# Performance work log

Measured on AMD Instinct MI355X. Metric: run time of the kernel, lower is better.

Reference implementation:

```python
import jax, jax.numpy as jnp
import numpy as np

NUM_NODES = 50000
NUM_EDGES = 800000
NUM_GRAPHS = 100
NODES_PER_GRAPH = 500
K = 250  # ceil(0.5 * NODES_PER_GRAPH), TopKPooling ratio=0.5
D = 64
OUT = 10


def gcn_conv(x, edge_index, W, b, num_nodes):
    """PyG GCNConv: add self-loops, symmetric D^-1/2 (A+I) D^-1/2 (x @ W) + b."""
    h = x @ W  # [N, Dout]
    loop = jnp.arange(num_nodes)
    row = jnp.concatenate([edge_index[0], loop])  # sources
    col = jnp.concatenate([edge_index[1], loop])  # targets
    deg = jax.ops.segment_sum(jnp.ones_like(col, dtype=h.dtype), col,
                              num_segments=num_nodes)
    dis = jnp.where(deg > 0, jax.lax.rsqrt(jnp.maximum(deg, 1e-12)), 0.0)
    norm = dis[row] * dis[col]                      # [E+N]
    msgs = h[row] * norm[:, None]                   # gather + scale (memory bound)
    out = jax.ops.segment_sum(msgs, col, num_segments=num_nodes)
    return out + b


def setup_inputs() -> dict:
    key = jax.random.key(0)
    ks = jax.random.split(key, 8)
    x = jax.random.normal(ks[0], (NUM_NODES, D), jnp.float32)
    edge_index = jax.random.randint(ks[1], (2, NUM_EDGES), 0, NUM_NODES)
    batch = jnp.arange(NUM_NODES) // NODES_PER_GRAPH  # contiguous equal graphs
    s = 1.0 / np.sqrt(D)
    W0 = jax.random.uniform(ks[2], (D, D), jnp.float32, -s, s)
    b0 = jnp.zeros((D,), jnp.float32)
    W1 = jax.random.uniform(ks[3], (D, D), jnp.float32, -s, s)
    b1 = jnp.zeros((D,), jnp.float32)
    pool_w = jax.random.uniform(ks[4], (D,), jnp.float32, -s, s)
    W_lin = jax.random.uniform(ks[5], (D, OUT), jnp.float32, -s, s)
    b_lin = jnp.zeros((OUT,), jnp.float32)
    return {"x": x, "edge_index": edge_index, "batch": batch,
            "W0": W0, "b0": b0, "W1": W1, "b1": b1,
            "pool_w": pool_w, "W_lin": W_lin, "b_lin": b_lin}


def reference(x, edge_index, batch, W0, b0, W1, b1, pool_w, W_lin, b_lin):
    # NOTE: zip(convs, pools) runs only 2 iterations -> 2 convs, 1 pool.
    x = jax.nn.relu(gcn_conv(x, edge_index, W0, b0, NUM_NODES))
    x = jax.nn.relu(gcn_conv(x, edge_index, W1, b1, NUM_NODES))
    # TopKPooling: score = tanh((x . w) / ||w||), keep top-K per graph,
    # kept features are scaled by their score.
    score = jnp.tanh((x @ pool_w) / jnp.linalg.norm(pool_w))  # [N]
    score_g = score.reshape(NUM_GRAPHS, NODES_PER_GRAPH)
    top_s, top_i = jax.lax.top_k(score_g, K)                  # [G, K]
    gidx = (top_i + jnp.arange(NUM_GRAPHS)[:, None] * NODES_PER_GRAPH).reshape(-1)
    x_pool = x[gidx] * top_s.reshape(-1, 1)                   # [G*K, D]
    # global_mean_pool: each pooled graph has exactly K nodes
    pooled = x_pool.reshape(NUM_GRAPHS, K, D).mean(axis=1)    # [G, D]
    logits = pooled @ W_lin + b_lin                           # [G, OUT]
    return jax.nn.log_softmax(logits, axis=1)
```

## Files before the change

kernel.cpp:

```cpp
#include <hip/hip_runtime.h>
#include <hip/hip_bf16.h>
#include <math.h>

#define NODES 50000
#define EDGES 800000
#define GRAPHS 100
#define NPG 500
#define KTOP 250
#define DIM 64
#define OUTC 10
#define SLOTS 64
#define GROWS 32
#define NBKT 196
#define BCAP 5120

#define WS_FLAG      0u
#define WS_INVNORM   4u
#define WS_W1F       512u
#define WS_B0F       16896u
#define WS_B1F       17152u
#define WS_PWF       17408u
#define WS_WLF       17664u
#define WS_BLF       20224u
#define WS_CURS      20480u
#define WS_CNT       21504u
#define WS_DIS       221696u
#define WS_SCORE     421888u
#define WS_EBUF      622080u
#define WS_SLOT      4636160u
#define WS_H1B       11036160u
#define WS_H2B       17436160u
#define WS_X2        23836160u

__device__ __forceinline__ float bf16_bits_to_f32(unsigned short u) {
    return __uint_as_float(((unsigned int)u) << 16);
}
__device__ __forceinline__ float bf16_lo(unsigned int u) {
    return __uint_as_float(u << 16);
}
__device__ __forceinline__ float bf16_hi(unsigned int u) {
    return __uint_as_float(u & 0xffff0000u);
}
__device__ __forceinline__ unsigned short f32_to_bf16(float f) {
    unsigned int u = __float_as_uint(f);
    u += 0x7fffu + ((u >> 16) & 1u);
    return (unsigned short)(u >> 16);
}
__device__ __forceinline__ unsigned int f32_sortable(float f) {
    unsigned int b = __float_as_uint(f);
    return (b & 0x80000000u) ? ~b : (b | 0x80000000u);
}

__global__ __launch_bounds__(512) void k_bucket(const int* __restrict__ ei,
        const void* w0p, const void* b0p, const void* w1p, const void* b1p,
        const void* pwp, const void* wlp, const void* blp, char* __restrict__ ws) {
    int bid = blockIdx.x, t = threadIdx.x;
    if (bid < NBKT) {
        __shared__ int hist[NBKT];
        __shared__ int base[NBKT];
        if (t < NBKT) hist[t] = 0;
        __syncthreads();
        int e0 = bid * 4096;
        int rr[8], cc[8], loc[8];
        long be = (long)e0 + (long)t * 8;
        if (be + 8 <= EDGES) {
            int4 ra = ((const int4*)(ei + e0))[t * 2];
            int4 rb = ((const int4*)(ei + e0))[t * 2 + 1];
            int4 ca = ((const int4*)(ei + EDGES + e0))[t * 2];
            int4 cb = ((const int4*)(ei + EDGES + e0))[t * 2 + 1];
            rr[0] = ra.x; rr[1] = ra.y; rr[2] = ra.z; rr[3] = ra.w;
            rr[4] = rb.x; rr[5] = rb.y; rr[6] = rb.z; rr[7] = rb.w;
            cc[0] = ca.x; cc[1] = ca.y; cc[2] = ca.z; cc[3] = ca.w;
            cc[4] = cb.x; cc[5] = cb.y; cc[6] = cb.z; cc[7] = cb.w;
        } else {
#pragma unroll
            for (int j = 0; j < 8; j++) {
                long e = be + j;
                if (e < EDGES) { rr[j] = ei[e]; cc[j] = ei[EDGES + e]; }
                else cc[j] = -1;
            }
        }
#pragma unroll
        for (int j = 0; j < 8; j++)
            if (cc[j] >= 0) loc[j] = atomicAdd(&hist[cc[j] >> 8], 1);
        __syncthreads();
        if (t < NBKT) base[t] = atomicAdd((int*)(ws + WS_CURS) + t, hist[t]);
        __syncthreads();
        unsigned int* eb = (unsigned int*)(ws + WS_EBUF);
#pragma unroll
        for (int j = 0; j < 8; j++) {
            if (cc[j] >= 0) {
                int b = cc[j] >> 8;
                int o = base[b] + loc[j];
                if (o < BCAP)
                    eb[b * BCAP + o] =
                        ((unsigned int)(cc[j] & 255) << 16) | (unsigned int)rr[j];
            }
        }
        return;
    }
    __shared__ int red_sh[512];
    __shared__ float fred[64];
    const unsigned short* u16 = (const unsigned short*)w0p;
    int c = 0;
    for (int i = t; i < 4096; i += 512) {
        float v = bf16_bits_to_f32(u16[i]);
        float av = fabsf(v);
        if (v == 0.0f || (av >= 1e-9f && av <= 0.25f)) c++;
    }
    red_sh[t] = c;
    __syncthreads();
    for (int s = 256; s > 0; s >>= 1) {
        if (t < s) red_sh[t] += red_sh[t + s];
        __syncthreads();
    }
    int flag = (red_sh[0] >= 3686) ? 1 : 0;
    if (t == 0) *(int*)(ws + WS_FLAG) = flag;
    const void* srcs[6] = {w1p, b0p, b1p, pwp, wlp, blp};
    const int   ns[6]   = {4096, 64, 64, 64, 640, 10};
    const unsigned int dsts[6] = {WS_W1F, WS_B0F, WS_B1F, WS_PWF, WS_WLF, WS_BLF};
    for (int a = 0; a < 6; a++) {
        float* dst = (float*)(ws + dsts[a]);
        if (flag) {
            const unsigned short* sp = (const unsigned short*)srcs[a];
            for (int i = t; i < ns[a]; i += 512) dst[i] = bf16_bits_to_f32(sp[i]);
        } else {
            const float* sp = (const float*)srcs[a];
            for (int i = t; i < ns[a]; i += 512) dst[i] = sp[i];
        }
    }
    __syncthreads();
    if (t < 64) {
        float w = ((float*)(ws + WS_PWF))[t];
        fred[t] = w * w;
    }
    __syncthreads();
    if (t == 0) {
        float ssum = 0.f;
        for (int i = 0; i < 64; i++) ssum += fred[i];
        *(float*)(ws + WS_INVNORM) = rsqrtf(ssum);
    }
}

__global__ __launch_bounds__(1024) void k_build(char* __restrict__ ws) {
    __shared__ unsigned short slsh[256 * SLOTS];
    __shared__ int cl_cnt[256];
    int b = blockIdx.x, t = threadIdx.x;
    if (t < 256) cl_cnt[t] = 0;
    __syncthreads();
    int n = ((const int*)(ws + WS_CURS))[b];
    if (n > BCAP) n = BCAP;
    const unsigned int* eb = (const unsigned int*)(ws + WS_EBUF) + b * BCAP;
    for (int i = t; i < n; i += 1024) {
        unsigned int u = eb[i];
        int cl = u >> 16;
        int r = u & 0xffffu;
        int p = atomicAdd(&cl_cnt[cl], 1);
        if (p < SLOTS) slsh[cl * SLOTS + p] = (unsigned short)r;
    }
    __syncthreads();
    uint4* dstv = (uint4*)((unsigned short*)(ws + WS_SLOT) + (b << 8) * SLOTS);
    const uint4* srcv = (const uint4*)slsh;
    for (int i = t; i < 2048; i += 1024) dstv[i] = srcv[i];
    if (t < 256) {
        int v = (b << 8) + t;
        if (v < NODES) {
            int cv = cl_cnt[t];
            ((int*)(ws + WS_CNT))[v] = cv;
            ((float*)(ws + WS_DIS))[v] = rsqrtf((float)(cv + 1));
        }
    }
}

__global__ __launch_bounds__(256) void k_gemm0(const void* __restrict__ xp,
        const void* __restrict__ w0p, char* __restrict__ ws,
        unsigned short* __restrict__ H1B) {
    __shared__ float Wsh[64 * 64];
    __shared__ float xsh[GROWS * 65];
    int bid = blockIdx.x, t = threadIdx.x;
    int flag = *(const int*)(ws + WS_FLAG);
    if (flag) {
        const unsigned short* wp = (const unsigned short*)w0p;
        for (int i = t; i < 4096; i += 256) Wsh[i] = bf16_bits_to_f32(wp[i]);
    } else {
        for (int i = t; i < 1024; i += 256)
            ((float4*)Wsh)[i] = ((const float4*)w0p)[i];
    }
    int row0 = bid * GROWS;
    for (int i = t; i < GROWS * 16; i += 256) {
        int r = i >> 4, q = i & 15;
        int gr = row0 + r;
        float4 v = {0.f, 0.f, 0.f, 0.f};
        if (gr < NODES) {
            if (flag) {
                ushort4 u = ((const ushort4*)xp)[gr * 16 + q];
                v.x = bf16_bits_to_f32(u.x); v.y = bf16_bits_to_f32(u.y);
                v.z = bf16_bits_to_f32(u.z); v.w = bf16_bits_to_f32(u.w);
            } else {
                v = ((const float4*)xp)[gr * 16 + q];
            }
        }
        float* xd = xsh + r * 65 + q * 4;
        xd[0] = v.x; xd[1] = v.y; xd[2] = v.z; xd[3] = v.w;
    }
    __syncthreads();
    int tc = t & 15, tr = t >> 4;
    int c0 = tc * 4, r0 = tr * 2;
    float4 a0 = {0, 0, 0, 0}, a1 = {0, 0, 0, 0};
#pragma unroll
    for (int k = 0; k < 64; k++) {
        float4 wv = *(const float4*)(Wsh + k * 64 + c0);
        float x0 = xsh[r0 * 65 + k];
        float x1 = xsh[(r0 + 1) * 65 + k];
        a0.x += wv.x * x0; a0.y += wv.y * x0; a0.z += wv.z * x0; a0.w += wv.w * x0;
        a1.x += wv.x * x1; a1.y += wv.y * x1; a1.z += wv.z * x1; a1.w += wv.w * x1;
    }
    int gr0 = row0 + r0;
    ushort4 s0, s1;
    s0.x = f32_to_bf16(a0.x); s0.y = f32_to_bf16(a0.y);
    s0.z = f32_to_bf16(a0.z); s0.w = f32_to_bf16(a0.w);
    s1.x = f32_to_bf16(a1.x); s1.y = f32_to_bf16(a1.y);
    s1.z = f32_to_bf16(a1.z); s1.w = f32_to_bf16(a1.w);
    if (gr0 < NODES)     *(ushort4*)(H1B + gr0 * 64 + c0) = s0;
    if (gr0 + 1 < NODES) *(ushort4*)(H1B + (gr0 + 1) * 64 + c0) = s1;
}

__device__ __forceinline__ void agg_core(const unsigned short* __restrict__ HB,
        const char* __restrict__ ws, int v, int eg, int dh,
        const float* bias, float4& olo, float4& ohi, float& dvo) {
    const int* cnt = (const int*)(ws + WS_CNT);
    const unsigned short* slot = (const unsigned short*)(ws + WS_SLOT) + v * SLOTS;
    const float* dis = (const float*)(ws + WS_DIS);
    int deg = cnt[v];
    if (deg > SLOTS) deg = SLOTS;
    float dv = dis[v];
    dvo = dv;
    float4 alo = {0, 0, 0, 0}, ahi = {0, 0, 0, 0};
    float4 blo = {0, 0, 0, 0}, bhi = {0, 0, 0, 0};
    if (eg == 0) {
        uint4 u = *(const uint4*)(HB + v * 64 + dh * 8);
        alo.x = bf16_lo(u.x) * dv; alo.y = bf16_hi(u.x) * dv;
        alo.z = bf16_lo(u.y) * dv; alo.w = bf16_hi(u.y) * dv;
        ahi.x = bf16_lo(u.z) * dv; ahi.y = bf16_hi(u.z) * dv;
        ahi.z = bf16_lo(u.w) * dv; ahi.w = bf16_hi(u.w) * dv;
    }
    int e = eg;
    for (; e + 8 < deg; e += 16) {
        int sA = slot[e], sB = slot[e + 8];
        float dA = dis[sA], dB = dis[sB];
        uint4 uA = *(const uint4*)(HB + sA * 64 + dh * 8);
        uint4 uB = *(const uint4*)(HB + sB * 64 + dh * 8);
        alo.x += bf16_lo(uA.x) * dA; alo.y += bf16_hi(uA.x) * dA;
        alo.z += bf16_lo(uA.y) * dA; alo.w += bf16_hi(uA.y) * dA;
        ahi.x += bf16_lo(uA.z) * dA; ahi.y += bf16_hi(uA.z) * dA;
        ahi.z += bf16_lo(uA.w) * dA; ahi.w += bf16_hi(uA.w) * dA;
        blo.x += bf16_lo(uB.x) * dB; blo.y += bf16_hi(uB.x) * dB;
        blo.z += bf16_lo(uB.y) * dB; blo.w += bf16_hi(uB.y) * dB;
        bhi.x += bf16_lo(uB.z) * dB; bhi.y += bf16_hi(uB.z) * dB;
        bhi.z += bf16_lo(uB.w) * dB; bhi.w += bf16_hi(uB.w) * dB;
    }
    if (e < deg) {
        int sA = slot[e];
        float dA = dis[sA];
        uint4 uA = *(const uint4*)(HB + sA * 64 + dh * 8);
        alo.x += bf16_lo(uA.x) * dA; alo.y += bf16_hi(uA.x) * dA;
        alo.z += bf16_lo(uA.y) * dA; alo.w += bf16_hi(uA.y) * dA;
        ahi.x += bf16_lo(uA.z) * dA; ahi.y += bf16_hi(uA.z) * dA;
        ahi.z += bf16_lo(uA.w) * dA; ahi.w += bf16_hi(uA.w) * dA;
    }
    alo.x += blo.x; alo.y += blo.y; alo.z += blo.z; alo.w += blo.w;
    ahi.x += bhi.x; ahi.y += bhi.y; ahi.z += bhi.z; ahi.w += bhi.w;
#pragma unroll
    for (int m = 8; m <= 32; m <<= 1) {
        alo.x += __shfl_xor(alo.x, m, 64); alo.y += __shfl_xor(alo.y, m, 64);
        alo.z += __shfl_xor(alo.z, m, 64); alo.w += __shfl_xor(alo.w, m, 64);
        ahi.x += __shfl_xor(ahi.x, m, 64); ahi.y += __shfl_xor(ahi.y, m, 64);
        ahi.z += __shfl_xor(ahi.z, m, 64); ahi.w += __shfl_xor(ahi.w, m, 64);
    }
    float4 b4a = *(const float4*)(bias + dh * 8);
    float4 b4b = *(const float4*)(bias + dh * 8 + 4);
    olo.x = fmaxf(alo.x * dv + b4a.x, 0.f);
    olo.y = fmaxf(alo.y * dv + b4a.y, 0.f);
    olo.z = fmaxf(alo.z * dv + b4a.z, 0.f);
    olo.w = fmaxf(alo.w * dv + b4a.w, 0.f);
    ohi.x = fmaxf(ahi.x * dv + b4b.x, 0.f);
    ohi.y = fmaxf(ahi.y * dv + b4b.y, 0.f);
    ohi.z = fmaxf(ahi.z * dv + b4b.z, 0.f);
    ohi.w = fmaxf(ahi.w * dv + b4b.w, 0.f);
}

__global__ __launch_bounds__(512) void k_agg1g(const unsigned short* __restrict__ H1B,
        char* __restrict__ ws, unsigned short* __restrict__ H2B) {
    __shared__ float Wsh[4096];
    int t = threadIdx.x;
    const float* W1F = (const float*)(ws + WS_W1F);
    for (int i = t; i < 4096; i += 512) {
        int k = i >> 6, cc = i & 63;
        int qp = (cc >> 2) ^ (k >> 3);
        Wsh[k * 64 + (qp << 2) + (cc & 3)] = W1F[i];
    }
    __syncthreads();
    int wv = t >> 6, lane = t & 63, eg = lane >> 3, dh = lane & 7;
    int v = blockIdx.x * 8 + wv;
    float4 olo, ohi;
    float dv;
    agg_core(H1B, ws, v, eg, dh, (const float*)(ws + WS_B0F), olo, ohi, dv);
    float av[8] = {olo.x, olo.y, olo.z, olo.w, ohi.x, ohi.y, ohi.z, ohi.w};
    float y[8] = {0.f, 0.f, 0.f, 0.f, 0.f, 0.f, 0.f, 0.f};
    const float* Wk = Wsh + dh * 512;
    int q0 = (((eg << 1)) ^ dh) << 2;
    int q1 = (((eg << 1) | 1) ^ dh) << 2;
#pragma unroll
    for (int j = 0; j < 8; j++) {
        float a = av[j];
        float4 w0 = *(const float4*)(Wk + j * 64 + q0);
        float4 w1 = *(const float4*)(Wk + j * 64 + q1);
        y[0] += a * w0.x; y[1] += a * w0.y; y[2] += a * w0.z; y[3] += a * w0.w;
        y[4] += a * w1.x; y[5] += a * w1.y; y[6] += a * w1.z; y[7] += a * w1.w;
    }
#pragma unroll
    for (int m = 1; m <= 4; m <<= 1) {
#pragma unroll
        for (int q = 0; q < 8; q++) y[q] += __shfl_xor(y[q], m, 64);
    }
    if (dh < 2) {
        ushort4 s;
        if (dh == 0) {
            s.x = f32_to_bf16(y[0] * dv); s.y = f32_to_bf16(y[1] * dv);
            s.z = f32_to_bf16(y[2] * dv); s.w = f32_to_bf16(y[3] * dv);
        } else {
            s.x = f32_to_bf16(y[4] * dv); s.y = f32_to_bf16(y[5] * dv);
            s.z = f32_to_bf16(y[6] * dv); s.w = f32_to_bf16(y[7] * dv);
        }
        *(ushort4*)(H2B + v * 64 + (eg << 3) + (dh << 2)) = s;
    }
}

__global__ __launch_bounds__(256) void k_agg2(const unsigned short* __restrict__ H2B,
        char* __restrict__ ws, float* __restrict__ X2) {
    int t = threadIdx.x;
    int g = t >> 3, dl = t & 7;
    int v = blockIdx.x * 32 + g;
    if (v >= NODES) return;
    int deg = ((const int*)(ws + WS_CNT))[v];
    if (deg > SLOTS) deg = SLOTS;
    float dv = ((const float*)(ws + WS_DIS))[v];
    const unsigned short* slot = (const unsigned short*)(ws + WS_SLOT) + v * SLOTS;
    const unsigned short* rb = H2B + dl * 8;
    uint4 u = *(const uint4*)(rb + v * 64);
    float a0 = bf16_lo(u.x), a1 = bf16_hi(u.x), a2 = bf16_lo(u.y), a3 = bf16_hi(u.y);
    float a4 = bf16_lo(u.z), a5 = bf16_hi(u.z), a6 = bf16_lo(u.w), a7 = bf16_hi(u.w);
    float b0 = 0.f, b1 = 0.f, b2 = 0.f, b3 = 0.f;
    float b4 = 0.f, b5 = 0.f, b6 = 0.f, b7 = 0.f;
    int e = 0;
    for (; e + 1 < deg; e += 2) {
        int sA = slot[e], sB = slot[e + 1];
        uint4 uA = *(const uint4*)(rb + sA * 64);
        uint4 uB = *(const uint4*)(rb + sB * 64);
        a0 += bf16_lo(uA.x); a1 += bf16_hi(uA.x);
        a2 += bf16_lo(uA.y); a3 += bf16_hi(uA.y);
        a4 += bf16_lo(uA.z); a5 += bf16_hi(uA.z);
        a6 += bf16_lo(uA.w); a7 += bf16_hi(uA.w);
        b0 += bf16_lo(uB.x); b1 += bf16_hi(uB.x);
        b2 += bf16_lo(uB.y); b3 += bf16_hi(uB.y);
        b4 += bf16_lo(uB.z); b5 += bf16_hi(uB.z);
        b6 += bf16_lo(uB.w); b7 += bf16_hi(uB.w);
    }
    if (e < deg) {
        int sA = slot[e];
        uint4 uA = *(const uint4*)(rb + sA * 64);
        a0 += bf16_lo(uA.x); a1 += bf16_hi(uA.x);
        a2 += bf16_lo(uA.y); a3 += bf16_hi(uA.y);
        a4 += bf16_lo(uA.z); a5 += bf16_hi(uA.z);
        a6 += bf16_lo(uA.w); a7 += bf16_hi(uA.w);
    }
    a0 += b0; a1 += b1; a2 += b2; a3 += b3;
    a4 += b4; a5 += b5; a6 += b6; a7 += b7;
    const float* bias = (const float*)(ws + WS_B1F) + dl * 8;
    float4 bb0 = *(const float4*)(bias);
    float4 bb1 = *(const float4*)(bias + 4);
    float4 o0, o1;
    o0.x = fmaxf(a0 * dv + bb0.x, 0.f);
    o0.y = fmaxf(a1 * dv + bb0.y, 0.f);
    o0.z = fmaxf(a2 * dv + bb0.z, 0.f);
    o0.w = fmaxf(a3 * dv + bb0.w, 0.f);
    o1.x = fmaxf(a4 * dv + bb1.x, 0.f);
    o1.y = fmaxf(a5 * dv + bb1.y, 0.f);
    o1.z = fmaxf(a6 * dv + bb1.z, 0.f);
    o1.w = fmaxf(a7 * dv + bb1.w, 0.f);
    *(float4*)(X2 + v * 64 + dl * 8) = o0;
    *(float4*)(X2 + v * 64 + dl * 8 + 4) = o1;
    const float* pw = (const float*)(ws + WS_PWF) + dl * 8;
    float4 pa = *(const float4*)(pw);
    float4 pb = *(const float4*)(pw + 4);
    float p = o0.x * pa.x + o0.y * pa.y + o0.z * pa.z + o0.w * pa.w
            + o1.x * pb.x + o1.y * pb.y + o1.z * pb.z + o1.w * pb.w;
    p += __shfl_xor(p, 1, 64);
    p += __shfl_xor(p, 2, 64);
    p += __shfl_xor(p, 4, 64);
    if (dl == 0) {
        float invn = *(const float*)(ws + WS_INVNORM);
        ((float*)(ws + WS_SCORE))[v] = tanhf(p * invn);
    }
}

template<int K, int J>
__device__ __forceinline__ void bstage(unsigned long long (&a)[8], int lane) {
    if constexpr (J >= 8) {
        constexpr int m = J >> 3;
#pragma unroll
        for (int s = 0; s < 8; s++) {
            unsigned long long other = __shfl_xor(a[s], m, 64);
            int e = (lane << 3) | s;
            bool keep_min = ((e & K) == 0) ^ ((lane & m) != 0);
            bool less = a[s] < other;
            a[s] = (keep_min == less) ? a[s] : other;
        }
    } else {
#pragma unroll
        for (int s = 0; s < 8; s++) {
            if ((s & J) == 0) {
                constexpr int j = J;
                int sp = s | j;
                int e = (lane << 3) | s;
                bool up = ((e & K) == 0);
                bool sw = up ? (a[s] > a[sp]) : (a[s] < a[sp]);
                if (sw) { unsigned long long tmp = a[s]; a[s] = a[sp]; a[sp] = tmp; }
            }
        }
    }
    if constexpr (J > 1) bstage<K, (J >> 1)>(a, lane);
}

__global__ __launch_bounds__(1024) void k_topk(char* __restrict__ ws,
        const float* __restrict__ X2, void* __restrict__ out) {
    __shared__ unsigned long long pairs[KTOP];
    __shared__ float part[1024];
    __shared__ float pool_sh[64];
    __shared__ float lsh[OUTC];
    int g = blockIdx.x, t = threadIdx.x;
    int wv = t >> 6, lane = t & 63;
    const float* sc = (const float*)(ws + WS_SCORE) + g * NPG;

    if (wv == 0) {
        unsigned long long a[8];
#pragma unroll
        for (int s = 0; s < 8; s++) {
            int e = (lane << 3) | s;
            if (e < NPG) {
                unsigned int key = ~f32_sortable(sc[e]);
                a[s] = ((unsigned long long)key << 32) | (unsigned int)e;
            } else {
                a[s] = 0xFFFFFFFFFFFFFFFFull;
            }
        }
        bstage<2, 1>(a, lane);
        bstage<4, 2>(a, lane);
        bstage<8, 4>(a, lane);
        bstage<16, 8>(a, lane);
        bstage<32, 16>(a, lane);
        bstage<64, 32>(a, lane);
        bstage<128, 64>(a, lane);
        bstage<256, 128>(a, lane);
        bstage<512, 256>(a, lane);
#pragma unroll
        for (int s = 0; s < 8; s++) {
            int r = (lane << 3) | s;
            if (r < KTOP) pairs[r] = a[s];
        }
    }
    __syncthreads();

    int d = lane;
    float acc = 0.f;
    for (int r = wv; r < KTOP; r += 16) {
        unsigned long long p = pairs[r];
        unsigned int u = ~(unsigned int)(p >> 32);
        unsigned int sbits = (u & 0x80000000u) ? (u ^ 0x80000000u) : ~u;
        float score = __uint_as_float(sbits);
        int idx = (int)(p & 0xFFFFFFFFu);
        acc += score * X2[(g * NPG + idx) * 64 + d];
    }
    part[t] = acc;
    __syncthreads();
    if (wv == 0) {
        float s = 0.f;
#pragma unroll
        for (int w = 0; w < 16; w++) s += part[w * 64 + d];
        pool_sh[d] = s * (1.0f / KTOP);
    }
    __syncthreads();
    if (t < 64) {
        float pd = pool_sh[t];
        const float* Wl = (const float*)(ws + WS_WLF);
        const float* bl = (const float*)(ws + WS_BLF);
        for (int o = 0; o < OUTC; o++) {
            float p = pd * Wl[t * OUTC + o];
            for (int s = 32; s > 0; s >>= 1) p += __shfl_down(p, s, 64);
            if (t == 0) lsh[o] = p + bl[o];
        }
        if (t == 0) {
            int flag = *(const int*)(ws + WS_FLAG);
            float mx = lsh[0];
            for (int o = 1; o < OUTC; o++) mx = fmaxf(mx, lsh[o]);
            float se = 0.f;
            for (int o = 0; o < OUTC; o++) se += expf(lsh[o] - mx);
            float lse = logf(se);
            for (int o = 0; o < OUTC; o++) {
                float vv = lsh[o] - mx - lse;
                if (flag) ((__hip_bfloat16*)out)[g * OUTC + o] = __float2bfloat16(vv);
                else      ((float*)out)[g * OUTC + o] = vv;
            }
        }
    }
}

extern "C" void kernel_launch(void* const* d_in, const int* in_sizes, int n_in,
                              void* d_out, int out_size, void* d_ws, size_t ws_size,
                              hipStream_t stream) {
    (void)in_sizes; (void)n_in; (void)out_size; (void)ws_size;
    char* ws = (char*)d_ws;
    const void* xp = d_in[0];
    const int* ei = (const int*)d_in[1];
    unsigned short* H1B = (unsigned short*)(ws + WS_H1B);
    unsigned short* H2B = (unsigned short*)(ws + WS_H2B);
    float* X2 = (float*)(ws + WS_X2);

    (void)hipMemsetAsync(ws + WS_CURS, 0, NBKT * sizeof(int), stream);
    k_bucket<<<NBKT + 1, 512, 0, stream>>>(ei, d_in[3], d_in[4], d_in[5],
                                           d_in[6], d_in[7], d_in[8], d_in[9], ws);
    k_build<<<NBKT, 1024, 0, stream>>>(ws);
    k_gemm0<<<1563, 256, 0, stream>>>(xp, d_in[3], ws, H1B);
    k_agg1g<<<6250, 512, 0, stream>>>(H1B, ws, H2B);
    k_agg2<<<1563, 256, 0, stream>>>(H2B, ws, X2);
    k_topk<<<100, 1024, 0, stream>>>(ws, X2, d_out);
}
```

Baseline: 137.1 us.

## Split fused layer-1 aggregation+GEMM into separate aggregation and tiled GEMM kernels

The fused k_agg1g kernel, which ran one wave per node with 8 edge-groups, shuffle reductions and a per-node W1 multiply, is replaced by two kernels. k_agg1 uses 8 threads per node with serial edge loops and writes a bf16 intermediate A1B. k_gemm1 then does a shared-memory tiled 32-row GEMM with W1 and scales by dis. This removes the shuffle reductions and per-block W1 reloads, and lets the gather use the same layout as k_agg2. In exchange it adds an extra kernel launch and a round trip of the 50000x64 bf16 intermediate through global memory.

```diff
diff --git a/kernel.cpp b/kernel.cpp
--- a/kernel.cpp
+++ b/kernel.cpp
@@ -31,6 +31,7 @@
 #define WS_H1B       11036160u
 #define WS_H2B       17436160u
 #define WS_X2        23836160u
+#define WS_A1B       WS_X2
 
 __device__ __forceinline__ float bf16_bits_to_f32(unsigned short u) {
     return __uint_as_float(((unsigned int)u) << 16);
@@ -225,114 +226,115 @@
     if (gr0 + 1 < NODES) *(ushort4*)(H1B + (gr0 + 1) * 64 + c0) = s1;
 }
 
-__device__ __forceinline__ void agg_core(const unsigned short* __restrict__ HB,
-        const char* __restrict__ ws, int v, int eg, int dh,
-        const float* bias, float4& olo, float4& ohi, float& dvo) {
-    const int* cnt = (const int*)(ws + WS_CNT);
+__global__ __launch_bounds__(256) void k_agg1(const unsigned short* __restrict__ H1B,
+        char* __restrict__ ws, unsigned short* __restrict__ A1B) {
+    int t = threadIdx.x;
+    int g = t >> 3, dl = t & 7;
+    int v = blockIdx.x * 32 + g;
+    if (v >= NODES) return;
+    int deg = ((const int*)(ws + WS_CNT))[v];
+    if (deg > SLOTS) deg = SLOTS;
+    const float* dis = (const float*)(ws + WS_DIS);
+    float dv = dis[v];
     const unsigned short* slot = (const unsigned short*)(ws + WS_SLOT) + v * SLOTS;
-    const float* dis = (const float*)(ws + WS_DIS);
-    int deg = cnt[v];
-    if (deg > SLOTS) deg = SLOTS;
-    float dv = dis[v];
-    dvo = dv;
-    float4 alo = {0, 0, 0, 0}, ahi = {0, 0, 0, 0};
-    float4 blo = {0, 0, 0, 0}, bhi = {0, 0, 0, 0};
-    if (eg == 0) {
-        uint4 u = *(const uint4*)(HB + v * 64 + dh * 8);
-        alo.x = bf16_lo(u.x) * dv; alo.y = bf16_hi(u.x) * dv;
-        alo.z = bf16_lo(u.y) * dv; alo.w = bf16_hi(u.y) * dv;
-        ahi.x = bf16_lo(u.z) * dv; ahi.y = bf16_hi(u.z) * dv;
-        ahi.z = bf16_lo(u.w) * dv; ahi.w = bf16_hi(u.w) * dv;
-    }
-    int e = eg;
-    for (; e + 8 < deg; e += 16) {
-        int sA = slot[e], sB = slot[e + 8];
+    const unsigned short* rb = H1B + dl * 8;
+    uint4 u = *(const uint4*)(rb + v * 64);
+    float a0 = bf16_lo(u.x) * dv, a1 = bf16_hi(u.x) * dv;
+    float a2 = bf16_lo(u.y) * dv, a3 = bf16_hi(u.y) * dv;
+    float a4 = bf16_lo(u.z) * dv, a5 = bf16_hi(u.z) * dv;
+    float a6 = bf16_lo(u.w) * dv, a7 = bf16_hi(u.w) * dv;
+    float b0 = 0.f, b1 = 0.f, b2 = 0.f, b3 = 0.f;
+    float b4 = 0.f, b5 = 0.f, b6 = 0.f, b7 = 0.f;
+    int e = 0;
+    for (; e + 1 < deg; e += 2) {
+        int sA = slot[e], sB = slot[e + 1];
         float dA = dis[sA], dB = dis[sB];
-        uint4 uA = *(const uint4*)(HB + sA * 64 + dh * 8);
-        uint4 uB = *(const uint4*)(HB + sB * 64 + dh * 8);
-        alo.x += bf16_lo(uA.x) * dA; alo.y += bf16_hi(uA.x) * dA;
-        alo.z += bf16_lo(uA.y) * dA; alo.w += bf16_hi(uA.y) * dA;
-        ahi.x += bf16_lo(uA.z) * dA; ahi.y += bf16_hi(uA.z) * dA;
-        ahi.z += bf16_lo(uA.w) * dA; ahi.w += bf16_hi(uA.w) * dA;
-        blo.x += bf16_lo(uB.x) * dB; blo.y += bf16_hi(uB.x) * dB;
-        blo.z += bf16_lo(uB.y) * dB; blo.w += bf16_hi(uB.y) * dB;
-        bhi.x += bf16_lo(uB.z) * dB; bhi.y += bf16_hi(uB.z) * dB;
-        bhi.z += bf16_lo(uB.w) * dB; bhi.w += bf16_hi(uB.w) * dB;
+        uint4 uA = *(const uint4*)(rb + sA * 64);
+        uint4 uB = *(const uint4*)(rb + sB * 64);
+        a0 += bf16_lo(uA.x) * dA; a1 += bf16_hi(uA.x) * dA;
+        a2 += bf16_lo(uA.y) * dA; a3 += bf16_hi(uA.y) * dA;
+        a4 += bf16_lo(uA.z) * dA; a5 += bf16_hi(uA.z) * dA;
+        a6 += bf16_lo(uA.w) * dA; a7 += bf16_hi(uA.w) * dA;
+        b0 += bf16_lo(uB.x) * dB; b1 += bf16_hi(uB.x) * dB;
+        b2 += bf16_lo(uB.y) * dB; b3 += bf16_hi(uB.y) * dB;
+        b4 += bf16_lo(uB.z) * dB; b5 += bf16_hi(uB.z) * dB;
+        b6 += bf16_lo(uB.w) * dB; b7 += bf16_hi(uB.w) * dB;
     }
     if (e < deg) {
         int sA = slot[e];
         float dA = dis[sA];
-        uint4 uA = *(const uint4*)(HB + sA * 64 + dh * 8);
-        alo.x += bf16_lo(uA.x) * dA; alo.y += bf16_hi(uA.x) * dA;
-        alo.z += bf16_lo(uA.y) * dA; alo.w += bf16_hi(uA.y) * dA;
-        ahi.x += bf16_lo(uA.z) * dA; ahi.y += bf16_hi(uA.z) * dA;
-        ahi.z += bf16_lo(uA.w) * dA; ahi.w += bf16_hi(uA.w) * dA;
-    }
-    alo.x += blo.x; alo.y += blo.y; alo.z += blo.z; alo.w += blo.w;
-    ahi.x += bhi.x; ahi.y += bhi.y; ahi.z += bhi.z; ahi.w += bhi.w;
-#pragma unroll
-    for (int m = 8; m <= 32; m <<= 1) {
-        alo.x += __shfl_xor(alo.x, m, 64); alo.y += __shfl_xor(alo.y, m, 64);
-        alo.z += __shfl_xor(alo.z, m, 64); alo.w += __shfl_xor(alo.w, m, 64);
-        ahi.x += __shfl_xor(ahi.x, m, 64); ahi.y += __shfl_xor(ahi.y, m, 64);
-        ahi.z += __shfl_xor(ahi.z, m, 64); ahi.w += __shfl_xor(ahi.w, m, 64);
-    }
-    float4 b4a = *(const float4*)(bias + dh * 8);
-    float4 b4b = *(const float4*)(bias + dh * 8 + 4);
-    olo.x = fmaxf(alo.x * dv + b4a.x, 0.f);
-    olo.y = fmaxf(alo.y * dv + b4a.y, 0.f);
-    olo.z = fmaxf(alo.z * dv + b4a.z, 0.f);
-    olo.w = fmaxf(alo.w * dv + b4a.w, 0.f);
-    ohi.x = fmaxf(ahi.x * dv + b4b.x, 0.f);
-    ohi.y = fmaxf(ahi.y * dv + b4b.y, 0.f);
-    ohi.z = fmaxf(ahi.z * dv + b4b.z, 0.f);
-    ohi.w = fmaxf(ahi.w * dv + b4b.w, 0.f);
-}
-
-__global__ __launch_bounds__(512) void k_agg1g(const unsigned short* __restrict__ H1B,
+        uint4 uA = *(const uint4*)(rb + sA * 64);
+        a0 += bf16_lo(uA.x) * dA; a1 += bf16_hi(uA.x) * dA;
+        a2 += bf16_lo(uA.y) * dA; a3 += bf16_hi(uA.y) * dA;
+        a4 += bf16_lo(uA.z) * dA; a5 += bf16_hi(uA.z) * dA;
+        a6 += bf16_lo(uA.w) * dA; a7 += bf16_hi(uA.w) * dA;
+    }
+    a0 += b0; a1 += b1; a2 += b2; a3 += b3;
+    a4 += b4; a5 += b5; a6 += b6; a7 += b7;
+    const float* bias = (const float*)(ws + WS_B0F) + dl * 8;
+    float4 bb0 = *(const float4*)(bias);
+    float4 bb1 = *(const float4*)(bias + 4);
+    ushort4 s0, s1;
+    s0.x = f32_to_bf16(fmaxf(a0 * dv + bb0.x, 0.f));
+    s0.y = f32_to_bf16(fmaxf(a1 * dv + bb0.y, 0.f));
+    s0.z = f32_to_bf16(fmaxf(a2 * dv + bb0.z, 0.f));
+    s0.w = f32_to_bf16(fmaxf(a3 * dv + bb0.w, 0.f));
+    s1.x = f32_to_bf16(fmaxf(a4 * dv + bb1.x, 0.f));
+    s1.y = f32_to_bf16(fmaxf(a5 * dv + bb1.y, 0.f));
+    s1.z = f32_to_bf16(fmaxf(a6 * dv + bb1.z, 0.f));
+    s1.w = f32_to_bf16(fmaxf(a7 * dv + bb1.w, 0.f));
+    *(ushort4*)(A1B + v * 64 + dl * 8) = s0;
+    *(ushort4*)(A1B + v * 64 + dl * 8 + 4) = s1;
+}
+
+__global__ __launch_bounds__(256) void k_gemm1(const unsigned short* __restrict__ A1B,
         char* __restrict__ ws, unsigned short* __restrict__ H2B) {
-    __shared__ float Wsh[4096];
-    int t = threadIdx.x;
+    __shared__ float Wsh[64 * 64];
+    __shared__ float xsh[GROWS * 65];
+    int bid = blockIdx.x, t = threadIdx.x;
     const float* W1F = (const float*)(ws + WS_W1F);
-    for (int i = t; i < 4096; i += 512) {
-        int k = i >> 6, cc = i & 63;
-        int qp = (cc >> 2) ^ (k >> 3);
-        Wsh[k * 64 + (qp << 2) + (cc & 3)] = W1F[i];
-    }
-    __syncthreads();
-    int wv = t >> 6, lane = t & 63, eg = lane >> 3, dh = lane & 7;
-    int v = blockIdx.x * 8 + wv;
-    float4 olo, ohi;
-    float dv;
-    agg_core(H1B, ws, v, eg, dh, (const float*)(ws + WS_B0F), olo, ohi, dv);
-    float av[8] = {olo.x, olo.y, olo.z, olo.w, ohi.x, ohi.y, ohi.z, ohi.w};
-    float y[8] = {0.f, 0.f, 0.f, 0.f, 0.f, 0.f, 0.f, 0.f};
-    const float* Wk = Wsh + dh * 512;
-    int q0 = (((eg << 1)) ^ dh) << 2;
-    int q1 = (((eg << 1) | 1) ^ dh) << 2;
-#pragma unroll
-    for (int j = 0; j < 8; j++) {
-        float a = av[j];
-        float4 w0 = *(const float4*)(Wk + j * 64 + q0);
-        float4 w1 = *(const float4*)(Wk + j * 64 + q1);
-        y[0] += a * w0.x; y[1] += a * w0.y; y[2] += a * w0.z; y[3] += a * w0.w;
-        y[4] += a * w1.x; y[5] += a * w1.y; y[6] += a * w1.z; y[7] += a * w1.w;
-    }
-#pragma unroll
-    for (int m = 1; m <= 4; m <<= 1) {
-#pragma unroll
-        for (int q = 0; q < 8; q++) y[q] += __shfl_xor(y[q], m, 64);
-    }
-    if (dh < 2) {
+    for (int i = t; i < 1024; i += 256)
+        ((float4*)Wsh)[i] = ((const float4*)W1F)[i];
+    int row0 = bid * GROWS;
+    for (int i = t; i < GROWS * 16; i += 256) {
+        int r = i >> 4, q = i & 15;
+        int gr = row0 + r;
+        float4 v = {0.f, 0.f, 0.f, 0.f};
+        if (gr < NODES) {
+            ushort4 u = ((const ushort4*)A1B)[gr * 16 + q];
+            v.x = bf16_bits_to_f32(u.x); v.y = bf16_bits_to_f32(u.y);
+            v.z = bf16_bits_to_f32(u.z); v.w = bf16_bits_to_f32(u.w);
+        }
+        float* xd = xsh + r * 65 + q * 4;
+        xd[0] = v.x; xd[1] = v.y; xd[2] = v.z; xd[3] = v.w;
+    }
+    __syncthreads();
+    int tc = t & 15, tr = t >> 4;
+    int c0 = tc * 4, r0 = tr * 2;
+    float4 a0 = {0, 0, 0, 0}, a1 = {0, 0, 0, 0};
+#pragma unroll
+    for (int k = 0; k < 64; k++) {
+        float4 wv = *(const float4*)(Wsh + k * 64 + c0);
+        float x0 = xsh[r0 * 65 + k];
+        float x1 = xsh[(r0 + 1) * 65 + k];
+        a0.x += wv.x * x0; a0.y += wv.y * x0; a0.z += wv.z * x0; a0.w += wv.w * x0;
+        a1.x += wv.x * x1; a1.y += wv.y * x1; a1.z += wv.z * x1; a1.w += wv.w * x1;
+    }
+    int gr0 = row0 + r0;
+    const float* dis = (const float*)(ws + WS_DIS);
+    if (gr0 < NODES) {
+        float d = dis[gr0];
         ushort4 s;
-        if (dh == 0) {
-            s.x = f32_to_bf16(y[0] * dv); s.y = f32_to_bf16(y[1] * dv);
-            s.z = f32_to_bf16(y[2] * dv); s.w = f32_to_bf16(y[3] * dv);
-        } else {
-            s.x = f32_to_bf16(y[4] * dv); s.y = f32_to_bf16(y[5] * dv);
-            s.z = f32_to_bf16(y[6] * dv); s.w = f32_to_bf16(y[7] * dv);
-        }
-        *(ushort4*)(H2B + v * 64 + (eg << 3) + (dh << 2)) = s;
+        s.x = f32_to_bf16(a0.x * d); s.y = f32_to_bf16(a0.y * d);
+        s.z = f32_to_bf16(a0.z * d); s.w = f32_to_bf16(a0.w * d);
+        *(ushort4*)(H2B + gr0 * 64 + c0) = s;
+    }
+    if (gr0 + 1 < NODES) {
+        float d = dis[gr0 + 1];
+        ushort4 s;
+        s.x = f32_to_bf16(a1.x * d); s.y = f32_to_bf16(a1.y * d);
+        s.z = f32_to_bf16(a1.z * d); s.w = f32_to_bf16(a1.w * d);
+        *(ushort4*)(H2B + (gr0 + 1) * 64 + c0) = s;
     }
 }
 
@@ -524,6 +526,7 @@
     const int* ei = (const int*)d_in[1];
     unsigned short* H1B = (unsigned short*)(ws + WS_H1B);
     unsigned short* H2B = (unsigned short*)(ws + WS_H2B);
+    unsigned short* A1B = (unsigned short*)(ws + WS_A1B);
     float* X2 = (float*)(ws + WS_X2);
 
     (void)hipMemsetAsync(ws + WS_CURS, 0, NBKT * sizeof(int), stream);
@@ -531,7 +534,8 @@
                                            d_in[6], d_in[7], d_in[8], d_in[9], ws);
     k_build<<<NBKT, 1024, 0, stream>>>(ws);
     k_gemm0<<<1563, 256, 0, stream>>>(xp, d_in[3], ws, H1B);
-    k_agg1g<<<6250, 512, 0, stream>>>(H1B, ws, H2B);
+    k_agg1<<<1563, 256, 0, stream>>>(H1B, ws, A1B);
+    k_gemm1<<<1563, 256, 0, stream>>>(A1B, ws, H2B);
     k_agg2<<<1563, 256, 0, stream>>>(H2B, ws, X2);
     k_topk<<<100, 1024, 0, stream>>>(ws, X2, d_out);
 }
```

New measurement: 135.0 us. No clear change (-1.5%).
